# Kernel tuning notes

Measured on AMD Instinct MI355X. Metric: run time of the kernel, lower is better.

Reference implementation:

```python
import jax, jax.numpy as jnp
import numpy as np

B, N, GEO, CLS = 32, 1024, 4, 28
F0 = GEO + CLS          # 32
F1 = F0 * 2             # 64
F2 = F0 * 4             # 128
EPS = 1e-5


def _lin(x, W, b):
    return x @ W.T + b


def _bn(x, g, b):
    # torch BatchNorm1d(element_num) on [B, N, F]: channel dim is N,
    # normalize over (batch, feature) with biased variance (training mode).
    m = x.mean(axis=(0, 2), keepdims=True)
    v = ((x - m) ** 2).mean(axis=(0, 2), keepdims=True)
    return g[None, :, None] * (x - m) * jax.lax.rsqrt(v + EPS) + b[None, :, None]


def _relation(x, Wu, bu, psi, phi, wr):
    # Vectorized form of the triple python loop:
    #   S[b,i,j] = psi*phi * <x_i, x_j>, diagonal excluded
    #   out_i   = wr * (sum_j S[b,i,j] * relu(unary(x_j))) / N + x_i
    n = x.shape[1]
    U = jax.nn.relu(_lin(x, Wu, bu))                       # [B,N,F2]
    S = (psi[0] * phi[0]) * jnp.einsum('bnd,bmd->bnm', x, x)
    S = S * (1.0 - jnp.eye(n, dtype=x.dtype))              # mask i==j
    return wr[0] * (S @ U) / n + x


def setup_inputs() -> dict:
    key = jax.random.key(0)
    ks = iter(jax.random.split(key, 64))

    def W(o, i):
        return jax.random.normal(next(ks), (o, i), jnp.float32) * 0.02

    def bvec(o):
        return jnp.zeros((o,), jnp.float32)

    inp = {'input': jax.random.uniform(next(ks), (B, N, F0), jnp.float32)}
    inp.update(e1_W=W(F1, F0), e1_b=bvec(F1),
               bn1_g=jnp.ones((N,), jnp.float32), bn1_b=bvec(N),
               e2_W=W(F2, F1), e2_b=bvec(F2),
               bn2_g=jnp.ones((N,), jnp.float32), bn2_b=bvec(N),
               e3_W=W(F2, F2), e3_b=bvec(F2))
    for r in (1, 2, 3, 4):
        inp[f'r{r}_W'] = W(F2, F2)
        inp[f'r{r}_b'] = bvec(F2)
        inp[f'r{r}_psi'] = jax.random.uniform(next(ks), (1,), jnp.float32)
        inp[f'r{r}_phi'] = jax.random.uniform(next(ks), (1,), jnp.float32)
        inp[f'r{r}_wr'] = jax.random.uniform(next(ks), (1,), jnp.float32)
    inp.update(d1_W=W(F1, F2), d1_b=bvec(F1),
               dbn_g=jnp.ones((N,), jnp.float32), dbn_b=bvec(N),
               d2_W=W(F0, F1), d2_b=bvec(F0),
               bc_W=W(CLS, F0), bc_b=bvec(CLS),
               bg_W=W(GEO, F0), bg_b=bvec(GEO))
    return inp


def reference(input, e1_W, e1_b, bn1_g, bn1_b, e2_W, e2_b, bn2_g, bn2_b,
              e3_W, e3_b,
              r1_W, r1_b, r1_psi, r1_phi, r1_wr,
              r2_W, r2_b, r2_psi, r2_phi, r2_wr,
              r3_W, r3_b, r3_psi, r3_phi, r3_wr,
              r4_W, r4_b, r4_psi, r4_phi, r4_wr,
              d1_W, d1_b, dbn_g, dbn_b, d2_W, d2_b,
              bc_W, bc_b, bg_W, bg_b):
    out = jax.nn.relu(_bn(_lin(input, e1_W, e1_b), bn1_g, bn1_b))
    out = jax.nn.relu(_bn(_lin(out, e2_W, e2_b), bn2_g, bn2_b))
    enc = jax.nn.sigmoid(_lin(out, e3_W, e3_b))
    x = _relation(enc, r1_W, r1_b, r1_psi, r1_phi, r1_wr)
    x = _relation(x, r2_W, r2_b, r2_psi, r2_phi, r2_wr)
    x = _relation(x, r3_W, r3_b, r3_psi, r3_phi, r3_wr)
    x = _relation(x, r4_W, r4_b, r4_psi, r4_phi, r4_wr)
    out = jax.nn.relu(_bn(_lin(x, d1_W, d1_b), dbn_g, dbn_b))
    out = jax.nn.relu(_lin(out, d2_W, d2_b))
    syn_cls = _lin(out, bc_W, bc_b)
    syn_geo = _lin(out, bg_W, bg_b)
    return jnp.concatenate((syn_cls, syn_geo), axis=2)
```

## Files before the change

### kernel.cpp

```cpp
#include <hip/hip_runtime.h>
#include <hip/hip_bf16.h>


typedef __hip_bfloat16 bf16;
typedef unsigned short ushort_t;
typedef float v4f __attribute__((ext_vector_type(4)));
typedef short v8s __attribute__((ext_vector_type(8)));
#define MFMA_BF16 __builtin_amdgcn_mfma_f32_16x16x32_bf16

#define NB 32
#define NN 1024

__device__ __forceinline__ float ldin(const void* p, size_t i, int f32){
    return f32 ? ((const float*)p)[i] : __bfloat162float(((const bf16*)p)[i]);
}
__device__ __forceinline__ float bf2f(ushort_t u){
    return __uint_as_float((unsigned)u << 16);
}
__device__ __forceinline__ ushort_t f2bf(float v){
    bf16 h = __float2bfloat16(v);
    ushort_t s; __builtin_memcpy(&s, &h, 2);
    return s;
}
__device__ __forceinline__ void unpack8(uint4 v, float* f){
    f[0] = __uint_as_float(v.x << 16);
    f[1] = __uint_as_float(v.x & 0xffff0000u);
    f[2] = __uint_as_float(v.y << 16);
    f[3] = __uint_as_float(v.y & 0xffff0000u);
    f[4] = __uint_as_float(v.z << 16);
    f[5] = __uint_as_float(v.z & 0xffff0000u);
    f[6] = __uint_as_float(v.w << 16);
    f[7] = __uint_as_float(v.w & 0xffff0000u);
}

__device__ __forceinline__ int detect_dev(const void* inp){
    __shared__ int sflag;
    int t = threadIdx.x;
    if (t < 64){
        unsigned v = ((const unsigned*)inp)[t];
        unsigned long long m = __ballot((v & 0x80008000u) != 0u);
        if (t == 0) sflag = (__popcll(m) > 4) ? 1 : 0;
    }
    __syncthreads();
    return sflag;
}

struct PrepArgs {
    const void* w[11];
    int K[11], O[11], off[11];
};

__global__ __launch_bounds__(256) void k_prep(PrepArgs a, float* __restrict__ wpf,
                                              ushort_t* __restrict__ whi, ushort_t* __restrict__ wlo,
                                              const void* __restrict__ detin){
    int f32 = detect_dev(detin);
    int s = blockIdx.y;
    int idx = blockIdx.x*256 + threadIdx.x;
    if (s < 6){
        int K = a.K[s], O = a.O[s];
        if (idx >= K*O) return;
        int k = idx / O, j = idx - k*O;
        wpf[a.off[s] + idx] = ldin(a.w[s], (size_t)j*K + k, f32);
    } else {
        if (idx >= 16384) return;
        int n = idx >> 7, k = idx & 127;
        float v = ldin(a.w[s], (size_t)n*128 + k, f32);
        ushort_t h = f2bf(v);
        ushort_t l = f2bf(v - bf2f(h));
        int di = (s - 6)*16384 + ((k >> 3)*128 + n)*8 + (k & 7);
        whi[di] = h; wlo[di] = l;
    }
}

template<int K, int O, bool EXTIN>
__global__ __launch_bounds__(128) void k_bnlin(
    const void* __restrict__ xin, const float* __restrict__ Wt,
    const void* __restrict__ bias, const void* __restrict__ bng,
    const void* __restrict__ bnb, ushort_t* __restrict__ out,
    const void* __restrict__ detin)
{
    int f32 = detect_dev(detin);
    constexpr int BR  = O/16;
    constexpr int NBT = 32/BR;
    constexpr int G   = K/8;
    __shared__ __align__(16) float wt[K*O];
    __shared__ __align__(16) float xst[2][K*36];
    int t = threadIdx.x;
    int w = t >> 6, lane = t & 63;
    int n = blockIdx.x*2 + w;

    for (int i = t; i < K*O/4; i += 128)
        ((float4*)wt)[i] = ((const float4*)Wt)[i];
    for (int i = lane; i < 32*G; i += 64){
        int b = i / G, g = i - b*G;
        float f[8];
        if (EXTIN && f32){
            const float* src = (const float*)xin + ((size_t)b*NN + n)*K + g*8;
            float4 v0 = ((const float4*)src)[0];
            float4 v1 = ((const float4*)src)[1];
            f[0]=v0.x; f[1]=v0.y; f[2]=v0.z; f[3]=v0.w;
            f[4]=v1.x; f[5]=v1.y; f[6]=v1.z; f[7]=v1.w;
        } else {
            uint4 v = *(const uint4*)((const ushort_t*)xin + ((size_t)b*NN + n)*K + (size_t)g*8);
            unpack8(v, f);
        }
        #pragma unroll
        for (int j=0;j<8;j++) xst[w][(g*8+j)*36 + b] = f[j];
    }
    __syncthreads();

    int bt = lane % NBT, jt = lane / NBT;
    int b0 = bt*BR, j0 = jt*8;
    const float* xw = xst[w];
    float acc[BR][8];
    #pragma unroll
    for (int i=0;i<BR;i++)
        #pragma unroll
        for (int j=0;j<8;j++) acc[i][j] = 0.f;

    for (int k = 0; k < K; k++){
        float xv[BR], wv[8];
        #pragma unroll
        for (int i=0;i<BR;i+=4)
            *(float4*)&xv[i] = *(const float4*)&xw[k*36 + b0 + i];
        *(float4*)&wv[0] = *(const float4*)&wt[k*O + j0];
        *(float4*)&wv[4] = *(const float4*)&wt[k*O + j0 + 4];
        #pragma unroll
        for (int i=0;i<BR;i++)
            #pragma unroll
            for (int j=0;j<8;j++) acc[i][j] = fmaf(xv[i], wv[j], acc[i][j]);
    }

    float bj[8];
    #pragma unroll
    for (int j=0;j<8;j++) bj[j] = ldin(bias, j0+j, f32);
    float s1 = 0.f, s2 = 0.f;
    #pragma unroll
    for (int i=0;i<BR;i++)
        #pragma unroll
        for (int j=0;j<8;j++){
            float a = acc[i][j] + bj[j];
            acc[i][j] = a; s1 += a; s2 = fmaf(a, a, s2);
        }
    #pragma unroll
    for (int off = 32; off > 0; off >>= 1){
        s1 += __shfl_down(s1, off);
        s2 += __shfl_down(s2, off);
    }
    s1 = __shfl(s1, 0); s2 = __shfl(s2, 0);
    const float M = 32.f * O;
    float m  = s1 / M;
    float vv = s2 / M - m*m;
    float rs = rsqrtf(vv + 1e-5f);
    float gv = ldin(bng, n, f32), bv = ldin(bnb, n, f32);
    #pragma unroll
    for (int i=0;i<BR;i++){
        union { uint4 u; ushort_t s[8]; } pk;
        #pragma unroll
        for (int j=0;j<8;j++)
            pk.s[j] = f2bf(fmaxf(fmaf(gv*(acc[i][j]-m), rs, bv), 0.f));
        *(uint4*)(out + ((size_t)(b0+i)*NN + n)*O + j0) = pk.u;
    }
}


__device__ __forceinline__ void tail_stage_x(ushort_t* xs, ushort_t* xt,
                                             const float o[2][16],
                                             int w, int col, int quad){
    #pragma unroll
    for (int nt=0;nt<2;nt++){
        int n = w*32 + nt*16 + col;
        #pragma unroll
        for (int m=0;m<4;m++){
            union { uint2 u2; ushort_t s[4]; } pk;
            #pragma unroll
            for (int reg=0;reg<4;reg++){
                int r = m*16 + quad*4 + reg;
                ushort_t hv = f2bf(o[nt][m*4+reg]);
                xs[((n>>3)*64 + r)*8 + (n&7)] = hv;
                pk.s[reg] = hv;
            }
            *(uint2*)&xt[n*64 + m*16 + quad*4] = pk.u2;
        }
    }
}

__device__ __forceinline__ void tail_write_A(const ushort_t* xs, ushort_t* A,
                                             size_t row0, int t){
    uint4* dst = (uint4*)(A + row0*128);
    #pragma unroll
    for (int c = 0; c < 4; c++){
        int i = t + c*256;
        int r = i >> 4, kg = i & 15;
        dst[i] = *(const uint4*)&xs[(kg*64 + r)*8];
    }
}

__device__ __forceinline__ void tail_lin_relu_T(ushort_t* xs, ushort_t* xt,
    ushort_t* UT, const ushort_t* Whi, const ushort_t* Wlo, const void* bias,
    float* dvec, float* Tp,
    size_t row0, int b, int rbase, int t, int w, int col, int quad, int f32)
{
    if (t < 64){
        float s = 0.f;
        #pragma unroll 8
        for (int k=0;k<128;k++){
            float v = bf2f(xs[((k>>3)*64 + t)*8 + (k&7)]);
            s = fmaf(v, v, s);
        }
        dvec[row0 + t] = s;
    }
    v4f acc[4][2];
    #pragma unroll
    for (int m=0;m<4;m++)
        #pragma unroll
        for (int nt=0;nt<2;nt++) acc[m][nt] = (v4f){0.f,0.f,0.f,0.f};
    #pragma unroll
    for (int kt = 0; kt < 4; kt++){
        int kg = kt*4 + quad;
        v8s a[4], bh[2], bl[2];
        #pragma unroll
        for (int nt=0;nt<2;nt++){
            int n = w*32 + nt*16 + col;
            bh[nt] = *(const v8s*)&Whi[(kg*128 + n)*8];
            bl[nt] = *(const v8s*)&Wlo[(kg*128 + n)*8];
        }
        #pragma unroll
        for (int m=0;m<4;m++)
            a[m] = *(const v8s*)&xs[(kg*64 + m*16 + col)*8];
        #pragma unroll
        for (int m=0;m<4;m++)
            #pragma unroll
            for (int nt=0;nt<2;nt++){
                acc[m][nt] = MFMA_BF16(a[m], bh[nt], acc[m][nt], 0, 0, 0);
                acc[m][nt] = MFMA_BF16(a[m], bl[nt], acc[m][nt], 0, 0, 0);
            }
    }
    float u[2][16];
    #pragma unroll
    for (int nt=0;nt<2;nt++){
        int n = w*32 + nt*16 + col;
        float bn = ldin(bias, n, f32);
        #pragma unroll
        for (int m=0;m<4;m++)
            #pragma unroll
            for (int reg=0;reg<4;reg++)
                u[nt][m*4+reg] = fmaxf(acc[m][nt][reg] + bn, 0.f);
    }
    __syncthreads();
    #pragma unroll
    for (int nt=0;nt<2;nt++){
        int n = w*32 + nt*16 + col;
        #pragma unroll
        for (int m=0;m<4;m++){
            union { uint2 u2; ushort_t s[4]; } pk;
            #pragma unroll
            for (int reg=0;reg<4;reg++)
                pk.s[reg] = f2bf(u[nt][m*4+reg]);
            *(uint2*)&xs[n*64 + m*16 + quad*4] = pk.u2;
        }
    }
    __syncthreads();
    #pragma unroll
    for (int c = 0; c < 4; c++){
        int i = t + c*256;
        int n = i >> 3, sg = i & 7;
        *(uint4*)&UT[((size_t)b*128 + n)*1024 + rbase + sg*8] =
            *(const uint4*)&xs[n*64 + sg*8];
    }
    v4f tacc[4][4];
    #pragma unroll
    for (int m=0;m<4;m++)
        #pragma unroll
        for (int q=0;q<4;q++) tacc[m][q] = (v4f){0.f,0.f,0.f,0.f};
    int wn = (w & 1)*64, wc = (w >> 1)*64;
    #pragma unroll
    for (int kt = 0; kt < 2; kt++){
        int kg = kt*4 + quad;
        v8s a[4], bb[4];
        #pragma unroll
        for (int m=0;m<4;m++)
            a[m] = *(const v8s*)&xs[(wn + m*16 + col)*64 + kg*8];
        #pragma unroll
        for (int q=0;q<4;q++)
            bb[q] = *(const v8s*)&xt[(wc + q*16 + col)*64 + kg*8];
        #pragma unroll
        for (int m=0;m<4;m++)
            #pragma unroll
            for (int q=0;q<4;q++)
                tacc[m][q] = MFMA_BF16(a[m], bb[q], tacc[m][q], 0, 0, 0);
    }
    int s16 = (int)((row0 >> 6) & 15);
    float* dst = Tp + ((size_t)(s16*NB + b) << 14);
    #pragma unroll
    for (int m=0;m<4;m++)
        #pragma unroll
        for (int q=0;q<4;q++)
            #pragma unroll
            for (int reg=0;reg<4;reg++){
                int n = wn + m*16 + quad*4 + reg;
                int c = wc + q*16 + col;
                dst[n*128 + c] = tacc[m][q][reg];
            }
}

__global__ __launch_bounds__(256) void k_linfuse0(
    const ushort_t* __restrict__ xin,
    const ushort_t* __restrict__ W3h, const ushort_t* __restrict__ W3l,
    const void* __restrict__ b3,
    const ushort_t* __restrict__ W1h, const ushort_t* __restrict__ W1l,
    const void* __restrict__ b1,
    ushort_t* __restrict__ A, ushort_t* __restrict__ UT,
    float* __restrict__ dvec, float* __restrict__ Tp,
    const void* __restrict__ detin)
{
    __shared__ __align__(16) ushort_t xs[8192];
    __shared__ __align__(16) ushort_t xt[8192];
    int f32 = detect_dev(detin);
    int t = threadIdx.x;
    size_t row0 = (size_t)blockIdx.x * 64;
    int b = (int)(row0 >> 10), rbase = (int)(row0 & 1023);
    {
        const uint4* src = (const uint4*)(xin + row0*128);
        #pragma unroll
        for (int c = 0; c < 4; c++){
            int i = t + c*256;
            int r = i >> 4, kg = i & 15;
            *(uint4*)&xs[(kg*64 + r)*8] = src[i];
        }
    }
    __syncthreads();
    int w = t >> 6, lane = t & 63;
    int col = lane & 15, quad = lane >> 4;
    v4f acc[4][2];
    #pragma unroll
    for (int m=0;m<4;m++)
        #pragma unroll
        for (int nt=0;nt<2;nt++) acc[m][nt] = (v4f){0.f,0.f,0.f,0.f};
    #pragma unroll
    for (int kt = 0; kt < 4; kt++){
        int kg = kt*4 + quad;
        v8s a[4], bh[2], bl[2];
        #pragma unroll
        for (int nt=0;nt<2;nt++){
            int n = w*32 + nt*16 + col;
            bh[nt] = *(const v8s*)&W3h[(kg*128 + n)*8];
            bl[nt] = *(const v8s*)&W3l[(kg*128 + n)*8];
        }
        #pragma unroll
        for (int m=0;m<4;m++)
            a[m] = *(const v8s*)&xs[(kg*64 + m*16 + col)*8];
        #pragma unroll
        for (int m=0;m<4;m++)
            #pragma unroll
            for (int nt=0;nt<2;nt++){
                acc[m][nt] = MFMA_BF16(a[m], bh[nt], acc[m][nt], 0, 0, 0);
                acc[m][nt] = MFMA_BF16(a[m], bl[nt], acc[m][nt], 0, 0, 0);
            }
    }
    float o[2][16];
    #pragma unroll
    for (int nt=0;nt<2;nt++){
        int n = w*32 + nt*16 + col;
        float bn = ldin(b3, n, f32);
        #pragma unroll
        for (int m=0;m<4;m++)
            #pragma unroll
            for (int reg=0;reg<4;reg++){
                float v = acc[m][nt][reg] + bn;
                o[nt][m*4+reg] = 1.f/(1.f+expf(-v));
            }
    }
    __syncthreads();
    tail_stage_x(xs, xt, o, w, col, quad);
    __syncthreads();
    tail_write_A(xs, A, row0, t);
    tail_lin_relu_T(xs, xt, UT, W1h, W1l, b1, dvec, Tp,
                    row0, b, rbase, t, w, col, quad, f32);
}

__global__ __launch_bounds__(256) void k_tred(const float* __restrict__ Tp,
                                              ushort_t* __restrict__ Thi, ushort_t* __restrict__ Tlo){
    int i = blockIdx.x*256 + threadIdx.x;
    const size_t S = 524288;
    float s = 0.f;
    #pragma unroll
    for (int k = 0; k < 16; k++) s += Tp[(size_t)k*S + i];
    int bb = i >> 14, j = i & 16383;
    int n = j >> 7, c = j & 127;
    int di = (bb << 14) + ((c >> 3)*128 + n)*8 + (c & 7);
    ushort_t h = f2bf(s);
    Thi[di] = h;
    Tlo[di] = f2bf(s - bf2f(h));
}

template<int LAST>
__global__ __launch_bounds__(256) void k_relfuse(
    ushort_t* __restrict__ x, ushort_t* __restrict__ UT,
    const ushort_t* __restrict__ Thi, const ushort_t* __restrict__ Tlo,
    float* __restrict__ dvec,
    const void* __restrict__ psi, const void* __restrict__ phi, const void* __restrict__ wr,
    const ushort_t* __restrict__ Wnh, const ushort_t* __restrict__ Wnl,
    const void* __restrict__ bnext, float* __restrict__ Tp,
    const void* __restrict__ detin)
{
    __shared__ __align__(16) ushort_t xs[8192];
    __shared__ __align__(16) ushort_t xt[8192];
    int f32 = detect_dev(detin);
    int t = threadIdx.x;
    size_t row0 = (size_t)blockIdx.x * 64;
    int b = (int)(row0 >> 10), rbase = (int)(row0 & 1023);
    {
        const uint4* src = (const uint4*)(x + row0*128);
        #pragma unroll
        for (int c = 0; c < 4; c++){
            int i = t + c*256;
            int r = i >> 4, kg = i & 15;
            *(uint4*)&xs[(kg*64 + r)*8] = src[i];
        }
    }
    __syncthreads();
    float alpha = ldin(wr,0,f32) * ldin(psi,0,f32) * ldin(phi,0,f32) * (1.f/1024.f);
    int w = t >> 6, lane = t & 63;
    int col = lane & 15, quad = lane >> 4;
    const ushort_t* sh = Thi + ((size_t)b << 14);
    const ushort_t* sl = Tlo + ((size_t)b << 14);
    v4f acc[4][2];
    #pragma unroll
    for (int m=0;m<4;m++)
        #pragma unroll
        for (int nt=0;nt<2;nt++) acc[m][nt] = (v4f){0.f,0.f,0.f,0.f};
    #pragma unroll
    for (int kt = 0; kt < 4; kt++){
        int kg = kt*4 + quad;
        v8s a[4], bh[2], bl[2];
        #pragma unroll
        for (int nt=0;nt<2;nt++){
            int n = w*32 + nt*16 + col;
            bh[nt] = *(const v8s*)&sh[(kg*128 + n)*8];
            bl[nt] = *(const v8s*)&sl[(kg*128 + n)*8];
        }
        #pragma unroll
        for (int m=0;m<4;m++)
            a[m] = *(const v8s*)&xs[(kg*64 + m*16 + col)*8];
        #pragma unroll
        for (int m=0;m<4;m++)
            #pragma unroll
            for (int nt=0;nt<2;nt++){
                acc[m][nt] = MFMA_BF16(a[m], bh[nt], acc[m][nt], 0, 0, 0);
                acc[m][nt] = MFMA_BF16(a[m], bl[nt], acc[m][nt], 0, 0, 0);
            }
    }
    float o[2][16];
    #pragma unroll
    for (int m=0;m<4;m++){
        float4 d4 = *(const float4*)&dvec[row0 + m*16 + quad*4];
        const float* dr = (const float*)&d4;
        #pragma unroll
        for (int nt=0;nt<2;nt++){
            int n = w*32 + nt*16 + col;
            uint2 uu = *(const uint2*)&UT[((size_t)b*128 + n)*1024 + rbase + m*16 + quad*4];
            float uf[4];
            uf[0] = __uint_as_float(uu.x << 16);
            uf[1] = __uint_as_float(uu.x & 0xffff0000u);
            uf[2] = __uint_as_float(uu.y << 16);
            uf[3] = __uint_as_float(uu.y & 0xffff0000u);
            #pragma unroll
            for (int reg=0;reg<4;reg++){
                int r = m*16 + quad*4 + reg;
                float xv = bf2f(xs[((n>>3)*64 + r)*8 + (n&7)]);
                o[nt][m*4+reg] = fmaf(alpha, acc[m][nt][reg] - dr[reg]*uf[reg], xv);
            }
        }
    }
    __syncthreads();
    tail_stage_x(xs, xt, o, w, col, quad);
    __syncthreads();
    tail_write_A(xs, x, row0, t);
    if (!LAST)
        tail_lin_relu_T(xs, xt, UT, Wnh, Wnl, bnext, dvec, Tp,
                        row0, b, rbase, t, w, col, quad, f32);
}

__global__ __launch_bounds__(256) void k_dec2(
    const ushort_t* __restrict__ x,
    const float* __restrict__ W2t, const void* __restrict__ b2,
    const float* __restrict__ Wct, const void* __restrict__ bcb,
    const float* __restrict__ Wgt, const void* __restrict__ bgb,
    void* __restrict__ out, const void* __restrict__ detin)
{
    int f32 = detect_dev(detin);
    __shared__ __align__(16) float w2[64*32];
    __shared__ __align__(16) float wc[32*28];
    __shared__ __align__(16) float wg[32*4];
    __shared__ __align__(16) float xsd[8][64];
    __shared__ float hs[8][33];
    size_t row0 = (size_t)blockIdx.x * 8;
    int t = threadIdx.x;
    for (int i=t;i<512;i+=256)  ((float4*)w2)[i] = ((const float4*)W2t)[i];
    if (t < 224) ((float4*)wc)[t] = ((const float4*)Wct)[t];
    if (t < 32)  ((float4*)wg)[t] = ((const float4*)Wgt)[t];
    if (t < 64){
        int row = t >> 3, seg = t & 7;
        uint4 v = *(const uint4*)&x[(row0 + row)*64 + seg*8];
        float f[8]; unpack8(v, f);
        *(float4*)&xsd[row][seg*8]   = make_float4(f[0],f[1],f[2],f[3]);
        *(float4*)&xsd[row][seg*8+4] = make_float4(f[4],f[5],f[6],f[7]);
    }
    __syncthreads();
    int j = t & 31, r = t >> 5;
    float a = ldin(b2, j, f32);
    #pragma unroll 8
    for (int k=0;k<64;k++) a = fmaf(xsd[r][k], w2[k*32 + j], a);
    hs[r][j] = fmaxf(a, 0.f);
    __syncthreads();
    float o;
    if (j < 28){
        o = ldin(bcb, j, f32);
        #pragma unroll
        for (int k=0;k<32;k++) o = fmaf(hs[r][k], wc[k*28 + j], o);
    } else {
        int jj = j - 28;
        o = ldin(bgb, jj, f32);
        #pragma unroll
        for (int k=0;k<32;k++) o = fmaf(hs[r][k], wg[k*4 + jj], o);
    }
    size_t oi = (row0 + r)*32 + j;
    if (f32) ((float*)out)[oi] = o;
    else     ((ushort_t*)out)[oi] = f2bf(o);
}

enum { O_E1=0, O_E2=2048, O_D1=10240, O_D2=18432, O_BC=20480, O_BG=21376 };

extern "C" void kernel_launch(void* const* d_in, const int* in_sizes, int n_in,
                              void* d_out, int out_size, void* d_ws, size_t ws_size,
                              hipStream_t stream)
{
    (void)in_sizes; (void)n_in; (void)out_size; (void)ws_size;
    const void* input = d_in[0];
    const void* e1_W = d_in[1];  const void* e1_b = d_in[2];
    const void* bn1_g = d_in[3]; const void* bn1_b = d_in[4];
    const void* e2_W = d_in[5];  const void* e2_b = d_in[6];
    const void* bn2_g = d_in[7]; const void* bn2_b = d_in[8];
    const void* e3_W = d_in[9];  const void* e3_b = d_in[10];
    const void *rW[4], *rb[4], *rpsi[4], *rphi[4], *rwr[4];
    for (int r = 0; r < 4; r++){
        rW[r]   = d_in[11 + r*5 + 0];
        rb[r]   = d_in[11 + r*5 + 1];
        rpsi[r] = d_in[11 + r*5 + 2];
        rphi[r] = d_in[11 + r*5 + 3];
        rwr[r]  = d_in[11 + r*5 + 4];
    }
    const void* d1_W = d_in[31]; const void* d1_b = d_in[32];
    const void* dbn_g = d_in[33];const void* dbn_b = d_in[34];
    const void* d2_W = d_in[35]; const void* d2_b = d_in[36];
    const void* bc_W = d_in[37]; const void* bc_b = d_in[38];
    const void* bg_W = d_in[39]; const void* bg_b = d_in[40];

    float*    ws_f = (float*)d_ws;
    float*    wpf  = ws_f;
    float*    dd   = ws_f + 21504;
    ushort_t* whi  = (ushort_t*)(ws_f + 54272);
    ushort_t* wlo  = (ushort_t*)(ws_f + 95232);
    ushort_t* Thi  = (ushort_t*)(ws_f + 136192);
    ushort_t* Tlo  = (ushort_t*)(ws_f + 398336);
    float*    Tp   = ws_f + 660480;
    ushort_t* A    = (ushort_t*)(ws_f + 9049088);
    ushort_t* UT   = (ushort_t*)(ws_f + 11146240);
    ushort_t* E2   = (ushort_t*)(ws_f + 13243392);
    ushort_t* Cenc = A;
    ushort_t* Cdec = UT;

    PrepArgs pa;
    const void* srcs[11] = {e1_W, e2_W, d1_W, d2_W, bc_W, bg_W,
                            e3_W, rW[0], rW[1], rW[2], rW[3]};
    const int  Ks[11]   = {32,64,128,64,32,32, 128,128,128,128,128};
    const int  Os[11]   = {64,128,64,32,28,4,  128,128,128,128,128};
    const int  offs[11] = {O_E1,O_E2,O_D1,O_D2,O_BC,O_BG, 0,0,0,0,0};
    for (int i=0;i<11;i++){ pa.w[i]=srcs[i]; pa.K[i]=Ks[i]; pa.O[i]=Os[i]; pa.off[i]=offs[i]; }

    k_prep<<<dim3(64,11), 256, 0, stream>>>(pa, wpf, whi, wlo, input);
    k_bnlin<32,64,true><<<512, 128, 0, stream>>>(input, wpf+O_E1, e1_b, bn1_g, bn1_b, Cenc, input);
    k_bnlin<64,128,false><<<512, 128, 0, stream>>>(Cenc, wpf+O_E2, e2_b, bn2_g, bn2_b, E2, input);
    k_linfuse0<<<512, 256, 0, stream>>>(E2, whi, wlo, e3_b,
                                        whi + 16384, wlo + 16384, rb[0],
                                        A, UT, dd, Tp, input);

    for (int r = 0; r < 4; r++){
        k_tred<<<2048, 256, 0, stream>>>(Tp, Thi, Tlo);
        if (r < 3)
            k_relfuse<0><<<512, 256, 0, stream>>>(A, UT, Thi, Tlo, dd,
                rpsi[r], rphi[r], rwr[r],
                whi + (size_t)(2+r)*16384, wlo + (size_t)(2+r)*16384, rb[r+1], Tp, input);
        else
            k_relfuse<1><<<512, 256, 0, stream>>>(A, UT, Thi, Tlo, dd,
                rpsi[r], rphi[r], rwr[r], whi, wlo, rb[r], Tp, input);
    }

    k_bnlin<128,64,false><<<512, 128, 0, stream>>>(A, wpf+O_D1, d1_b, dbn_g, dbn_b, Cdec, input);
    k_dec2<<<4096, 256, 0, stream>>>(Cdec, wpf+O_D2, d2_b, wpf+O_BC, bc_b, wpf+O_BG, bg_b, d_out, input);
}
```

Baseline: 326.4 us.

## Store partial T sums in bf16 and make decoder grid persistent

The per-slice partial products Tp (x^T U per 64-row slice) are now written as bf16 in a transposed layout with packed 8-byte stores instead of fp32 scalars. A new reduction kernel sums 16 slices and writes the hi/lo split with 16-byte vector stores using far fewer threads. This halves the partial-sum traffic but rounds each partial to bf16 before summation, which loses precision. Separately, the final decoder kernel becomes a grid-stride loop over 512 blocks so the weight staging in shared memory is reused across tiles.

```diff
diff --git a/kernel.cpp b/kernel.cpp
--- a/kernel.cpp
+++ b/kernel.cpp
@@ -198,7 +198,7 @@
 
 __device__ __forceinline__ void tail_lin_relu_T(ushort_t* xs, ushort_t* xt,
     ushort_t* UT, const ushort_t* Whi, const ushort_t* Wlo, const void* bias,
-    float* dvec, float* Tp,
+    float* dvec, ushort_t* Tp,
     size_t row0, int b, int rbase, int t, int w, int col, int quad, int f32)
 {
     if (t < 64){
@@ -291,17 +291,18 @@
                 tacc[m][q] = MFMA_BF16(a[m], bb[q], tacc[m][q], 0, 0, 0);
     }
     int s16 = (int)((row0 >> 6) & 15);
-    float* dst = Tp + ((size_t)(s16*NB + b) << 14);
+    ushort_t* dst = Tp + ((size_t)(s16*NB + b) << 14);
     #pragma unroll
     for (int m=0;m<4;m++)
         #pragma unroll
-        for (int q=0;q<4;q++)
-            #pragma unroll
-            for (int reg=0;reg<4;reg++){
-                int n = wn + m*16 + quad*4 + reg;
-                int c = wc + q*16 + col;
-                dst[n*128 + c] = tacc[m][q][reg];
-            }
+        for (int q=0;q<4;q++){
+            int c = wc + q*16 + col;
+            union { uint2 u2; ushort_t s[4]; } pk;
+            #pragma unroll
+            for (int reg=0;reg<4;reg++)
+                pk.s[reg] = f2bf(tacc[m][q][reg]);
+            *(uint2*)&dst[c*128 + wn + m*16 + quad*4] = pk.u2;
+        }
 }
 
 __global__ __launch_bounds__(256) void k_linfuse0(
@@ -311,7 +312,7 @@
     const ushort_t* __restrict__ W1h, const ushort_t* __restrict__ W1l,
     const void* __restrict__ b1,
     ushort_t* __restrict__ A, ushort_t* __restrict__ UT,
-    float* __restrict__ dvec, float* __restrict__ Tp,
+    float* __restrict__ dvec, ushort_t* __restrict__ Tp,
     const void* __restrict__ detin)
 {
     __shared__ __align__(16) ushort_t xs[8192];
@@ -379,19 +380,30 @@
                     row0, b, rbase, t, w, col, quad, f32);
 }
 
-__global__ __launch_bounds__(256) void k_tred(const float* __restrict__ Tp,
-                                              ushort_t* __restrict__ Thi, ushort_t* __restrict__ Tlo){
-    int i = blockIdx.x*256 + threadIdx.x;
-    const size_t S = 524288;
-    float s = 0.f;
-    #pragma unroll
-    for (int k = 0; k < 16; k++) s += Tp[(size_t)k*S + i];
-    int bb = i >> 14, j = i & 16383;
-    int n = j >> 7, c = j & 127;
-    int di = (bb << 14) + ((c >> 3)*128 + n)*8 + (c & 7);
-    ushort_t h = f2bf(s);
-    Thi[di] = h;
-    Tlo[di] = f2bf(s - bf2f(h));
+__global__ __launch_bounds__(256) void k_tredb(const ushort_t* __restrict__ Tp,
+                                               ushort_t* __restrict__ Thi, ushort_t* __restrict__ Tlo){
+    int tau = blockIdx.x*256 + threadIdx.x;
+    int b = tau >> 11;
+    int j2 = tau & 2047;
+    int cg = j2 >> 7, n = j2 & 127;
+    float sum[8] = {0,0,0,0,0,0,0,0};
+    #pragma unroll
+    for (int s = 0; s < 16; s++){
+        const ushort_t* src = Tp + ((size_t)(s*NB + b) << 14) + cg*8*128 + n;
+        #pragma unroll
+        for (int cc = 0; cc < 8; cc++)
+            sum[cc] += bf2f(src[cc*128]);
+    }
+    union { uint4 u; ushort_t s[8]; } ph, pl;
+    #pragma unroll
+    for (int cc = 0; cc < 8; cc++){
+        ushort_t h = f2bf(sum[cc]);
+        ph.s[cc] = h;
+        pl.s[cc] = f2bf(sum[cc] - bf2f(h));
+    }
+    size_t di = ((size_t)b << 14) + ((size_t)cg*128 + n)*8;
+    *(uint4*)&Thi[di] = ph.u;
+    *(uint4*)&Tlo[di] = pl.u;
 }
 
 template<int LAST>
@@ -401,7 +413,7 @@
     float* __restrict__ dvec,
     const void* __restrict__ psi, const void* __restrict__ phi, const void* __restrict__ wr,
     const ushort_t* __restrict__ Wnh, const ushort_t* __restrict__ Wnl,
-    const void* __restrict__ bnext, float* __restrict__ Tp,
+    const void* __restrict__ bnext, ushort_t* __restrict__ Tp,
     const void* __restrict__ detin)
 {
     __shared__ __align__(16) ushort_t xs[8192];
@@ -495,39 +507,42 @@
     __shared__ __align__(16) float wg[32*4];
     __shared__ __align__(16) float xsd[8][64];
     __shared__ float hs[8][33];
-    size_t row0 = (size_t)blockIdx.x * 8;
     int t = threadIdx.x;
     for (int i=t;i<512;i+=256)  ((float4*)w2)[i] = ((const float4*)W2t)[i];
     if (t < 224) ((float4*)wc)[t] = ((const float4*)Wct)[t];
     if (t < 32)  ((float4*)wg)[t] = ((const float4*)Wgt)[t];
-    if (t < 64){
-        int row = t >> 3, seg = t & 7;
-        uint4 v = *(const uint4*)&x[(row0 + row)*64 + seg*8];
-        float f[8]; unpack8(v, f);
-        *(float4*)&xsd[row][seg*8]   = make_float4(f[0],f[1],f[2],f[3]);
-        *(float4*)&xsd[row][seg*8+4] = make_float4(f[4],f[5],f[6],f[7]);
-    }
-    __syncthreads();
     int j = t & 31, r = t >> 5;
-    float a = ldin(b2, j, f32);
-    #pragma unroll 8
-    for (int k=0;k<64;k++) a = fmaf(xsd[r][k], w2[k*32 + j], a);
-    hs[r][j] = fmaxf(a, 0.f);
-    __syncthreads();
-    float o;
-    if (j < 28){
-        o = ldin(bcb, j, f32);
-        #pragma unroll
-        for (int k=0;k<32;k++) o = fmaf(hs[r][k], wc[k*28 + j], o);
-    } else {
-        int jj = j - 28;
-        o = ldin(bgb, jj, f32);
-        #pragma unroll
-        for (int k=0;k<32;k++) o = fmaf(hs[r][k], wg[k*4 + jj], o);
-    }
-    size_t oi = (row0 + r)*32 + j;
-    if (f32) ((float*)out)[oi] = o;
-    else     ((ushort_t*)out)[oi] = f2bf(o);
+    for (int tile = blockIdx.x; tile < 4096; tile += 512){
+        size_t row0 = (size_t)tile * 8;
+        __syncthreads();
+        if (t < 64){
+            int row = t >> 3, seg = t & 7;
+            uint4 v = *(const uint4*)&x[(row0 + row)*64 + seg*8];
+            float f[8]; unpack8(v, f);
+            *(float4*)&xsd[row][seg*8]   = make_float4(f[0],f[1],f[2],f[3]);
+            *(float4*)&xsd[row][seg*8+4] = make_float4(f[4],f[5],f[6],f[7]);
+        }
+        __syncthreads();
+        float a = ldin(b2, j, f32);
+        #pragma unroll 8
+        for (int k=0;k<64;k++) a = fmaf(xsd[r][k], w2[k*32 + j], a);
+        hs[r][j] = fmaxf(a, 0.f);
+        __syncthreads();
+        float o;
+        if (j < 28){
+            o = ldin(bcb, j, f32);
+            #pragma unroll
+            for (int k=0;k<32;k++) o = fmaf(hs[r][k], wc[k*28 + j], o);
+        } else {
+            int jj = j - 28;
+            o = ldin(bgb, jj, f32);
+            #pragma unroll
+            for (int k=0;k<32;k++) o = fmaf(hs[r][k], wg[k*4 + jj], o);
+        }
+        size_t oi = (row0 + r)*32 + j;
+        if (f32) ((float*)out)[oi] = o;
+        else     ((ushort_t*)out)[oi] = f2bf(o);
+    }
 }
 
 enum { O_E1=0, O_E2=2048, O_D1=10240, O_D2=18432, O_BC=20480, O_BG=21376 };
@@ -564,10 +579,10 @@
     ushort_t* wlo  = (ushort_t*)(ws_f + 95232);
     ushort_t* Thi  = (ushort_t*)(ws_f + 136192);
     ushort_t* Tlo  = (ushort_t*)(ws_f + 398336);
-    float*    Tp   = ws_f + 660480;
-    ushort_t* A    = (ushort_t*)(ws_f + 9049088);
-    ushort_t* UT   = (ushort_t*)(ws_f + 11146240);
-    ushort_t* E2   = (ushort_t*)(ws_f + 13243392);
+    ushort_t* Tp   = (ushort_t*)(ws_f + 660480);
+    ushort_t* A    = (ushort_t*)(ws_f + 4854784);
+    ushort_t* UT   = (ushort_t*)(ws_f + 6951936);
+    ushort_t* E2   = (ushort_t*)(ws_f + 9049088);
     ushort_t* Cenc = A;
     ushort_t* Cdec = UT;
 
@@ -587,7 +602,7 @@
                                         A, UT, dd, Tp, input);
 
     for (int r = 0; r < 4; r++){
-        k_tred<<<2048, 256, 0, stream>>>(Tp, Thi, Tlo);
+        k_tredb<<<256, 256, 0, stream>>>(Tp, Thi, Tlo);
         if (r < 3)
             k_relfuse<0><<<512, 256, 0, stream>>>(A, UT, Thi, Tlo, dd,
                 rpsi[r], rphi[r], rwr[r],
@@ -598,5 +613,5 @@
     }
 
     k_bnlin<128,64,false><<<512, 128, 0, stream>>>(A, wpf+O_D1, d1_b, dbn_g, dbn_b, Cdec, input);
-    k_dec2<<<4096, 256, 0, stream>>>(Cdec, wpf+O_D2, d2_b, wpf+O_BC, bc_b, wpf+O_BG, bg_b, d_out, input);
-}
+    k_dec2<<<512, 256, 0, stream>>>(Cdec, wpf+O_D2, d2_b, wpf+O_BC, bc_b, wpf+O_BG, bg_b, d_out, input);
+}
```

New measurement: 320.0 us. About the same (-2.0%).
